# Kernel tuning notes

Hardware: AMD Instinct MI355X
Metric: run time of the kernel (lower is better)

## Reference

```python
import jax, jax.numpy as jnp
import numpy as np

N = 262144   # active voxel sites
C = 128      # channels (inplanes == outplanes)
K = 27       # 3^3 submanifold kernel offsets
EPS = 1e-4   # scn BatchNormalization default eps


def setup_inputs() -> dict:
    key = jax.random.key(0)
    ks = jax.random.split(key, 5)
    features = jax.random.normal(ks[0], (N, C), dtype=jnp.float32)
    nbr_idx = jax.random.randint(ks[1], (N, K), 0, N, dtype=jnp.int32)
    nbr_mask = jax.random.randint(ks[2], (N, K), 0, 2, dtype=jnp.int32)
    center = K // 2  # submanifold: center offset is always the site itself
    nbr_idx = nbr_idx.at[:, center].set(jnp.arange(N, dtype=jnp.int32))
    nbr_mask = nbr_mask.at[:, center].set(1)
    s = 1.0 / np.sqrt(K * C).astype(np.float32)
    W1 = jax.random.normal(ks[3], (K, C, C), dtype=jnp.float32) * s
    W2 = jax.random.normal(ks[4], (K, C, C), dtype=jnp.float32) * s
    bias1 = jnp.zeros((C,), jnp.float32)
    bias2 = jnp.zeros((C,), jnp.float32)
    gamma1 = jnp.ones((C,), jnp.float32)
    beta1 = jnp.zeros((C,), jnp.float32)
    gamma2 = jnp.ones((C,), jnp.float32)
    beta2 = jnp.zeros((C,), jnp.float32)
    return dict(features=features, nbr_idx=nbr_idx, nbr_mask=nbr_mask,
                gamma1=gamma1, beta1=beta1, W1=W1, bias1=bias1,
                gamma2=gamma2, beta2=beta2, W2=W2, bias2=bias2)


def _bn_relu(x, gamma, beta):
    # BatchNormReLU over active sites (training-mode batch stats)
    mu = jnp.mean(x, axis=0)
    var = jnp.mean(jnp.square(x - mu), axis=0)
    scale = gamma * jax.lax.rsqrt(var + EPS)
    return jax.nn.relu((x - mu) * scale + beta)


def _subm_conv(x, nbr_idx, nbr_mask, W, b):
    # Rulebook-based submanifold conv: for each of K offsets, gather the
    # active neighbor feature (masked) and apply that offset's [Cin,Cout] matmul.
    m = nbr_mask.astype(x.dtype)
    acc = jnp.broadcast_to(b, (x.shape[0], W.shape[2]))
    for k in range(K):  # fixed small unroll over kernel offsets
        g = x[nbr_idx[:, k]] * m[:, k:k + 1]   # [N, Cin]
        acc = acc + g @ W[k]                    # [N, Cout]
    return acc


def reference(features, nbr_idx, nbr_mask, gamma1, beta1, W1, bias1,
              gamma2, beta2, W2, bias2):
    h = _bn_relu(features, gamma1, beta1)
    h = _subm_conv(h, nbr_idx, nbr_mask, W1, bias1)
    h = _bn_relu(h, gamma2, beta2)
    h = _subm_conv(h, nbr_idx, nbr_mask, W2, bias2)
    return h + features  # AddTable residual
```

## Files before the change

### kernel.cpp

```cpp
#include <hip/hip_runtime.h>

#define NS 262144
#define NK 27

typedef float f32x4 __attribute__((ext_vector_type(4)));
typedef __bf16 bf16x8 __attribute__((ext_vector_type(8)));

__device__ __forceinline__ unsigned short f2bf(float f) {
  union { float f; unsigned int i; } c; c.f = f;
  unsigned int r = c.i + 0x7fffu + ((c.i >> 16) & 1u);
  return (unsigned short)(r >> 16);
}
__device__ __forceinline__ float bf2f(unsigned short u) {
  union { unsigned int i; float f; } c; c.i = ((unsigned int)u) << 16;
  return c.f;
}
__device__ __forceinline__ void async16(const void* gp, void* lp) {
  __builtin_amdgcn_global_load_lds((const __attribute__((address_space(1))) void*)gp,
                                   (__attribute__((address_space(3))) void*)lp, 16, 0, 0);
}

__global__ __launch_bounds__(256) void prep_idx_kernel(const int* __restrict__ nidx,
                                                       const int* __restrict__ nmask,
                                                       int* __restrict__ idx2t) {
  __shared__ int li[256 * NK];
  __shared__ int lm[256 * NK];
  const int t = threadIdx.x;
  const int sb = blockIdx.x * 256;
  for (int j = t; j < 256 * NK; j += 256) {
    li[j] = nidx[(size_t)sb * NK + j];
    lm[j] = nmask[(size_t)sb * NK + j];
  }
  __syncthreads();
  for (int k = 0; k < NK; ++k) {
    int m = lm[t * NK + k];
    int v = li[t * NK + k];
    idx2t[(size_t)k * NS + sb + t] = m ? v : NS;
  }
}

__global__ __launch_bounds__(256) void prep_w_kernel(const float* __restrict__ W1,
                                                     const float* __restrict__ W2,
                                                     unsigned short* __restrict__ Wt1,
                                                     unsigned short* __restrict__ Wt2) {
  const int b = blockIdx.x;
  const float* W = (b < NK) ? W1 : W2;
  unsigned short* Wt = (b < NK) ? Wt1 : Wt2;
  const int k = (b < NK) ? b : b - NK;
  __shared__ unsigned short tile[128 * 130];
  const int t = threadIdx.x;
  for (int j = t; j < 16384; j += 256) {
    int ci = j >> 7, co = j & 127;
    tile[ci * 130 + co] = f2bf(W[(size_t)k * 16384 + j]);
  }
  __syncthreads();
  for (int j = t; j < 16384; j += 256) {
    int co = j >> 7, ci = j & 127;
    Wt[(size_t)k * 16384 + j] = tile[ci * 130 + co];
  }
}

__global__ __launch_bounds__(256) void stats_kernel(const float* __restrict__ x,
                                                    float* __restrict__ ssum,
                                                    float* __restrict__ sssq) {
  const int t = threadIdx.x;
  const int c4 = (t & 31) * 4;
  const int rsub = t >> 5;
  const int rowend = blockIdx.x * 512 + 512;
  float s0 = 0, s1 = 0, s2 = 0, s3 = 0, q0 = 0, q1 = 0, q2 = 0, q3 = 0;
  for (int r = blockIdx.x * 512 + rsub; r < rowend; r += 8) {
    const float4 v = *(const float4*)&x[(size_t)r * 128 + c4];
    s0 += v.x; q0 += v.x * v.x;
    s1 += v.y; q1 += v.y * v.y;
    s2 += v.z; q2 += v.z * v.z;
    s3 += v.w; q3 += v.w * v.w;
  }
  __shared__ float red[256 * 8];
  red[t * 8 + 0] = s0; red[t * 8 + 1] = s1; red[t * 8 + 2] = s2; red[t * 8 + 3] = s3;
  red[t * 8 + 4] = q0; red[t * 8 + 5] = q1; red[t * 8 + 6] = q2; red[t * 8 + 7] = q3;
  __syncthreads();
  if (t < 32) {
    float a0 = 0, a1 = 0, a2 = 0, a3 = 0, b0 = 0, b1 = 0, b2 = 0, b3 = 0;
    for (int j = 0; j < 8; ++j) {
      const float* p = &red[(j * 32 + t) * 8];
      a0 += p[0]; a1 += p[1]; a2 += p[2]; a3 += p[3];
      b0 += p[4]; b1 += p[5]; b2 += p[6]; b3 += p[7];
    }
    atomicAdd(&ssum[t * 4 + 0], a0); atomicAdd(&ssum[t * 4 + 1], a1);
    atomicAdd(&ssum[t * 4 + 2], a2); atomicAdd(&ssum[t * 4 + 3], a3);
    atomicAdd(&sssq[t * 4 + 0], b0); atomicAdd(&sssq[t * 4 + 1], b1);
    atomicAdd(&sssq[t * 4 + 2], b2); atomicAdd(&sssq[t * 4 + 3], b3);
  }
}

__global__ __launch_bounds__(256) void apply_f32_kernel(const float* __restrict__ x,
    const float* __restrict__ ssum, const float* __restrict__ sssq,
    const float* __restrict__ gamma, const float* __restrict__ beta,
    unsigned short* __restrict__ hout) {
  const size_t base = ((size_t)blockIdx.x * 256 + threadIdx.x) * 8;
  const int c0 = (int)(base & 127);
  const float4 v0 = *(const float4*)&x[base];
  const float4 v1 = *(const float4*)&x[base + 4];
  const float vv[8] = {v0.x, v0.y, v0.z, v0.w, v1.x, v1.y, v1.z, v1.w};
  unsigned short o[8] __attribute__((aligned(16)));
  const float invN = 1.0f / (float)NS;
  #pragma unroll
  for (int j = 0; j < 8; ++j) {
    const int c = c0 + j;
    const float mean = ssum[c] * invN;
    const float var = sssq[c] * invN - mean * mean;
    const float sc = gamma[c] * rsqrtf(var + 1e-4f);
    const float t = (vv[j] - mean) * sc + beta[c];
    o[j] = f2bf(fmaxf(t, 0.0f));
  }
  *(int4*)&hout[base] = *(const int4*)o;
  if (blockIdx.x == 0 && threadIdx.x < 16) {
    int4 z; z.x = 0; z.y = 0; z.z = 0; z.w = 0;
    ((int4*)(hout + (size_t)NS * 128))[threadIdx.x] = z;
  }
}

__global__ __launch_bounds__(256) void apply_bf16_kernel(const unsigned short* __restrict__ x,
    const float* __restrict__ ssum, const float* __restrict__ sssq,
    const float* __restrict__ gamma, const float* __restrict__ beta,
    unsigned short* __restrict__ hout) {
  const size_t base = ((size_t)blockIdx.x * 256 + threadIdx.x) * 8;
  const int c0 = (int)(base & 127);
  unsigned short in[8] __attribute__((aligned(16)));
  *(int4*)in = *(const int4*)&x[base];
  unsigned short o[8] __attribute__((aligned(16)));
  const float invN = 1.0f / (float)NS;
  #pragma unroll
  for (int j = 0; j < 8; ++j) {
    const int c = c0 + j;
    const float mean = ssum[c] * invN;
    const float var = sssq[c] * invN - mean * mean;
    const float sc = gamma[c] * rsqrtf(var + 1e-4f);
    const float t = (bf2f(in[j]) - mean) * sc + beta[c];
    o[j] = f2bf(fmaxf(t, 0.0f));
  }
  *(int4*)&hout[base] = *(const int4*)o;
}


#define WAITV(N) asm volatile("s_waitcnt vmcnt(" #N ")" ::: "memory")
#define SBAR() do { __builtin_amdgcn_sched_barrier(0); __builtin_amdgcn_s_barrier(); \
                    __builtin_amdgcn_sched_barrier(0); } while (0)
#define ROT() do { int _t = b0; b0 = b1; b1 = b2; b2 = _t; } while (0)

#define LOAD_ROWS(KK, D0, D1) do {                                                   \
    D0 = idx2t[(size_t)(KK) * NS + sb + wave * 16 + rsel];                           \
    D1 = idx2t[(size_t)(KK) * NS + sb + 64 + wave * 16 + rsel];                      \
  } while (0)

#define STAGE_U(BS, KK, QQ, R0, R1) do {                                             \
    const unsigned short* ga0 = h + (((size_t)(R0)) << 7) + ((QQ) << 5) + (gch << 3);\
    async16(ga0, &A_lds[(BS) + (wave << 9)]);                                        \
    const unsigned short* gb0 = Wt + (((size_t)(KK)) << 14) +                        \
        ((wave * 16 + rsel) << 7) + ((QQ) << 5) + (gch << 3);                        \
    async16(gb0, &B_lds[(BS) + (wave << 9)]);                                        \
    const unsigned short* ga1 = h + (((size_t)(R1)) << 7) + ((QQ) << 5) + (gch << 3);\
    async16(ga1, &A_lds[(BS) + 2048 + (wave << 9)]);                                 \
    const unsigned short* gb1 = Wt + (((size_t)(KK)) << 14) +                        \
        ((64 + wave * 16 + rsel) << 7) + ((QQ) << 5) + (gch << 3);                   \
    async16(gb1, &B_lds[(BS) + 2048 + (wave << 9)]);                                 \
  } while (0)

#define COMPUTE_U(BS) do {                                                           \
    bf16x8 af[4], bfr[4];                                                            \
    _Pragma("unroll")                                                                \
    for (int mi = 0; mi < 4; ++mi)                                                   \
      af[mi] = *(const bf16x8*)&A_lds[(BS) + ((wm * 64 + mi * 16 + i16) << 5) + (slotc << 3)]; \
    _Pragma("unroll")                                                                \
    for (int ni = 0; ni < 4; ++ni)                                                   \
      bfr[ni] = *(const bf16x8*)&B_lds[(BS) + ((wn * 64 + ni * 16 + i16) << 5) + (slotc << 3)]; \
    __builtin_amdgcn_s_setprio(1);                                                   \
    _Pragma("unroll")                                                                \
    for (int mi = 0; mi < 4; ++mi)                                                   \
      _Pragma("unroll")                                                              \
      for (int ni = 0; ni < 4; ++ni)                                                 \
        acc[mi][ni] = __builtin_amdgcn_mfma_f32_16x16x32_bf16(af[mi], bfr[ni], acc[mi][ni], 0, 0, 0); \
    __builtin_amdgcn_s_setprio(0);                                                   \
  } while (0)

template <bool FIRST>
__global__ __launch_bounds__(256, 3) void conv_kernel(
    const unsigned short* __restrict__ h,
    const int* __restrict__ idx2t,
    const unsigned short* __restrict__ Wt,
    const float* __restrict__ bias,
    unsigned short* __restrict__ out_bf,
    float* __restrict__ ssum, float* __restrict__ sssq,
    const float* __restrict__ resid,
    float* __restrict__ outf) {
  __shared__ unsigned short A_lds[3 * 4096];
  __shared__ unsigned short B_lds[3 * 4096];
  const int tid = threadIdx.x;
  const int wave = tid >> 6, lane = tid & 63;
  const int wm = wave >> 1, wn = wave & 1;
  const int i16 = lane & 15, quad = lane >> 4;
  const int rsel = lane >> 2;
  const int gch = (lane & 3) ^ ((lane >> 3) & 3);
  const int slotc = quad ^ ((i16 >> 1) & 3);
  const int sb = blockIdx.x << 7;

  f32x4 acc[4][4];
  #pragma unroll
  for (int a = 0; a < 4; ++a)
    #pragma unroll
    for (int b = 0; b < 4; ++b) { acc[a][b][0] = 0.f; acc[a][b][1] = 0.f; acc[a][b][2] = 0.f; acc[a][b][3] = 0.f; }

  int rE0, rE1, rO0, rO1;
  LOAD_ROWS(0, rE0, rE1);
  LOAD_ROWS(1, rO0, rO1);
  int b0 = 0, b1 = 4096, b2 = 8192;
  STAGE_U(0, 0, 0, rE0, rE1);
  STAGE_U(4096, 0, 1, rE0, rE1);

  #pragma unroll 1
  for (int kk = 0; kk < 26; kk += 2) {
    STAGE_U(b2, kk, 2, rE0, rE1);                       WAITV(8);  SBAR(); COMPUTE_U(b0); SBAR(); ROT();
    STAGE_U(b2, kk, 3, rE0, rE1); LOAD_ROWS(kk + 2, rE0, rE1);
                                                        WAITV(10); SBAR(); COMPUTE_U(b0); SBAR(); ROT();
    STAGE_U(b2, kk + 1, 0, rO0, rO1);                   WAITV(10); SBAR(); COMPUTE_U(b0); SBAR(); ROT();
    STAGE_U(b2, kk + 1, 1, rO0, rO1);                   WAITV(8);  SBAR(); COMPUTE_U(b0); SBAR(); ROT();

    STAGE_U(b2, kk + 1, 2, rO0, rO1);                   WAITV(8);  SBAR(); COMPUTE_U(b0); SBAR(); ROT();
    { const int k3 = (kk + 3 > 26) ? 26 : kk + 3;
      STAGE_U(b2, kk + 1, 3, rO0, rO1); LOAD_ROWS(k3, rO0, rO1); }
                                                        WAITV(10); SBAR(); COMPUTE_U(b0); SBAR(); ROT();
    STAGE_U(b2, kk + 2, 0, rE0, rE1);                   WAITV(10); SBAR(); COMPUTE_U(b0); SBAR(); ROT();
    STAGE_U(b2, kk + 2, 1, rE0, rE1);                   WAITV(8);  SBAR(); COMPUTE_U(b0); SBAR(); ROT();
  }
  STAGE_U(b2, 26, 2, rE0, rE1);                         WAITV(8);  SBAR(); COMPUTE_U(b0); SBAR(); ROT();
  STAGE_U(b2, 26, 3, rE0, rE1);                         WAITV(8);  SBAR(); COMPUTE_U(b0); SBAR(); ROT();
                                                        WAITV(4);  SBAR(); COMPUTE_U(b0); SBAR(); ROT();
                                                        WAITV(0);  SBAR(); COMPUTE_U(b0); SBAR();

  if (FIRST) {
    float cs[4], cq[4];
    #pragma unroll
    for (int ni = 0; ni < 4; ++ni) {
      const int col = wn * 64 + ni * 16 + i16;
      const float bv = bias[col];
      float s = 0.f, q = 0.f;
      #pragma unroll
      for (int mi = 0; mi < 4; ++mi) {
        const int rowb = sb + wm * 64 + mi * 16 + quad * 4;
        #pragma unroll
        for (int i = 0; i < 4; ++i) {
          const float v = acc[mi][ni][i] + bv;
          out_bf[(size_t)(rowb + i) * 128 + col] = f2bf(v);
          s += v; q += v * v;
        }
      }
      cs[ni] = s; cq[ni] = q;
    }
    #pragma unroll
    for (int ni = 0; ni < 4; ++ni) {
      cs[ni] += __shfl_xor(cs[ni], 16); cs[ni] += __shfl_xor(cs[ni], 32);
      cq[ni] += __shfl_xor(cq[ni], 16); cq[ni] += __shfl_xor(cq[ni], 32);
    }
    __syncthreads();
    float* red = (float*)A_lds;
    if (wm == 1 && quad == 0) {
      #pragma unroll
      for (int ni = 0; ni < 4; ++ni) {
        const int col = wn * 64 + ni * 16 + i16;
        red[col] = cs[ni]; red[128 + col] = cq[ni];
      }
    }
    __syncthreads();
    if (wm == 0 && quad == 0) {
      #pragma unroll
      for (int ni = 0; ni < 4; ++ni) {
        const int col = wn * 64 + ni * 16 + i16;
        atomicAdd(&ssum[col], cs[ni] + red[col]);
        atomicAdd(&sssq[col], cq[ni] + red[128 + col]);
      }
    }
  } else {
    #pragma unroll
    for (int ni = 0; ni < 4; ++ni) {
      const int col = wn * 64 + ni * 16 + i16;
      const float bv = bias[col];
      #pragma unroll
      for (int mi = 0; mi < 4; ++mi) {
        const int rowb = sb + wm * 64 + mi * 16 + quad * 4;
        #pragma unroll
        for (int i = 0; i < 4; ++i) {
          const size_t o = (size_t)(rowb + i) * 128 + col;
          outf[o] = acc[mi][ni][i] + bv + resid[o];
        }
      }
    }
  }
}

extern "C" void kernel_launch(void* const* d_in, const int* in_sizes, int n_in,
                              void* d_out, int out_size, void* d_ws, size_t ws_size,
                              hipStream_t stream) {
  const float* features = (const float*)d_in[0];
  const int* nbr_idx    = (const int*)d_in[1];
  const int* nbr_mask   = (const int*)d_in[2];
  const float* gamma1   = (const float*)d_in[3];
  const float* beta1    = (const float*)d_in[4];
  const float* W1       = (const float*)d_in[5];
  const float* bias1    = (const float*)d_in[6];
  const float* gamma2   = (const float*)d_in[7];
  const float* beta2    = (const float*)d_in[8];
  const float* W2       = (const float*)d_in[9];
  const float* bias2    = (const float*)d_in[10];

  char* ws = (char*)d_ws;
  size_t off = 0;
  unsigned short* h = (unsigned short*)(ws + off); off += (size_t)(NS + 1) * 128 * 2;
  unsigned short* out1 = (unsigned short*)(ws + off); off += (size_t)NS * 128 * 2;
  int* idx2t = (int*)(ws + off); off += (size_t)NK * NS * 4;
  unsigned short* Wt1 = (unsigned short*)(ws + off); off += (size_t)NK * 128 * 128 * 2;
  unsigned short* Wt2 = (unsigned short*)(ws + off); off += (size_t)NK * 128 * 128 * 2;
  float* stats = (float*)(ws + off); off += 4 * 128 * 4;
  float* sum1 = stats, *ssq1 = stats + 128, *sum2 = stats + 256, *ssq2 = stats + 384;

  hipMemsetAsync(stats, 0, 4 * 128 * 4, stream);
  prep_idx_kernel<<<NS / 256, 256, 0, stream>>>(nbr_idx, nbr_mask, idx2t);
  prep_w_kernel<<<2 * NK, 256, 0, stream>>>(W1, W2, Wt1, Wt2);
  stats_kernel<<<NS / 512, 256, 0, stream>>>(features, sum1, ssq1);
  apply_f32_kernel<<<(NS * 128) / 2048, 256, 0, stream>>>(features, sum1, ssq1, gamma1, beta1, h);
  conv_kernel<true><<<NS / 128, 256, 0, stream>>>(h, idx2t, Wt1, bias1, out1, sum2, ssq2, nullptr, nullptr);
  apply_bf16_kernel<<<(NS * 128) / 2048, 256, 0, stream>>>(out1, sum2, ssq2, gamma2, beta2, h);
  conv_kernel<false><<<NS / 128, 256, 0, stream>>>(h, idx2t, Wt2, bias2, nullptr, nullptr, nullptr,
                                                   features, (float*)d_out);
}
```

Measured before the change: 943.6 us.

## Use one barrier per pipeline stage and issue staging before compute

Restructures the triple-buffered gather-GEMM loop so each stage waits for its own loads, takes a single barrier, issues the next async global-to-LDS stage, then computes on the current buffer. The second barrier per step goes away and row-index loads are issued just in time, which also lowers the vmcnt thresholds. Scheduling barriers pin the prologue issue order. This cuts barrier overhead and lets loads overlap the MFMA work, but it depends on the triple-buffer rotation keeping the buffer being written distinct from those being read.

Result: no change. 937.0 us (-0.7%).

```diff
diff --git a/kernel.cpp b/kernel.cpp
--- a/kernel.cpp
+++ b/kernel.cpp
@@ -143,7 +143,8 @@
 }
 
 
-#define WAITV(N) asm volatile("s_waitcnt vmcnt(" #N ")" ::: "memory")
+#define WAITV_(N) asm volatile("s_waitcnt vmcnt(" #N ")" ::: "memory")
+#define WAITV(N) WAITV_(N)
 #define SBAR() do { __builtin_amdgcn_sched_barrier(0); __builtin_amdgcn_s_barrier(); \
                     __builtin_amdgcn_sched_barrier(0); } while (0)
 #define ROT() do { int _t = b0; b0 = b1; b1 = b2; b2 = _t; } while (0)
@@ -212,30 +213,30 @@
 
   int rE0, rE1, rO0, rO1;
   LOAD_ROWS(0, rE0, rE1);
-  LOAD_ROWS(1, rO0, rO1);
+  __builtin_amdgcn_sched_barrier(0);
   int b0 = 0, b1 = 4096, b2 = 8192;
   STAGE_U(0, 0, 0, rE0, rE1);
+  __builtin_amdgcn_sched_barrier(0);
   STAGE_U(4096, 0, 1, rE0, rE1);
+  __builtin_amdgcn_sched_barrier(0);
 
   #pragma unroll 1
   for (int kk = 0; kk < 26; kk += 2) {
-    STAGE_U(b2, kk, 2, rE0, rE1);                       WAITV(8);  SBAR(); COMPUTE_U(b0); SBAR(); ROT();
-    STAGE_U(b2, kk, 3, rE0, rE1); LOAD_ROWS(kk + 2, rE0, rE1);
-                                                        WAITV(10); SBAR(); COMPUTE_U(b0); SBAR(); ROT();
-    STAGE_U(b2, kk + 1, 0, rO0, rO1);                   WAITV(10); SBAR(); COMPUTE_U(b0); SBAR(); ROT();
-    STAGE_U(b2, kk + 1, 1, rO0, rO1);                   WAITV(8);  SBAR(); COMPUTE_U(b0); SBAR(); ROT();
-
-    STAGE_U(b2, kk + 1, 2, rO0, rO1);                   WAITV(8);  SBAR(); COMPUTE_U(b0); SBAR(); ROT();
-    { const int k3 = (kk + 3 > 26) ? 26 : kk + 3;
-      STAGE_U(b2, kk + 1, 3, rO0, rO1); LOAD_ROWS(k3, rO0, rO1); }
-                                                        WAITV(10); SBAR(); COMPUTE_U(b0); SBAR(); ROT();
-    STAGE_U(b2, kk + 2, 0, rE0, rE1);                   WAITV(10); SBAR(); COMPUTE_U(b0); SBAR(); ROT();
-    STAGE_U(b2, kk + 2, 1, rE0, rE1);                   WAITV(8);  SBAR(); COMPUTE_U(b0); SBAR(); ROT();
-  }
-  STAGE_U(b2, 26, 2, rE0, rE1);                         WAITV(8);  SBAR(); COMPUTE_U(b0); SBAR(); ROT();
-  STAGE_U(b2, 26, 3, rE0, rE1);                         WAITV(8);  SBAR(); COMPUTE_U(b0); SBAR(); ROT();
-                                                        WAITV(4);  SBAR(); COMPUTE_U(b0); SBAR(); ROT();
-                                                        WAITV(0);  SBAR(); COMPUTE_U(b0); SBAR();
+    WAITV(4); SBAR(); STAGE_U(b2, kk, 2, rE0, rE1);     COMPUTE_U(b0); ROT();
+    WAITV(4); SBAR(); LOAD_ROWS(kk + 1, rO0, rO1);
+                      STAGE_U(b2, kk, 3, rE0, rE1);     COMPUTE_U(b0); ROT();
+    WAITV(6); SBAR(); STAGE_U(b2, kk + 1, 0, rO0, rO1); COMPUTE_U(b0); ROT();
+    WAITV(4); SBAR(); STAGE_U(b2, kk + 1, 1, rO0, rO1); COMPUTE_U(b0); ROT();
+    WAITV(4); SBAR(); STAGE_U(b2, kk + 1, 2, rO0, rO1); COMPUTE_U(b0); ROT();
+    WAITV(4); SBAR(); LOAD_ROWS(kk + 2, rE0, rE1);
+                      STAGE_U(b2, kk + 1, 3, rO0, rO1); COMPUTE_U(b0); ROT();
+    WAITV(6); SBAR(); STAGE_U(b2, kk + 2, 0, rE0, rE1); COMPUTE_U(b0); ROT();
+    WAITV(4); SBAR(); STAGE_U(b2, kk + 2, 1, rE0, rE1); COMPUTE_U(b0); ROT();
+  }
+  WAITV(4); SBAR(); STAGE_U(b2, 26, 2, rE0, rE1); COMPUTE_U(b0); ROT();
+  WAITV(4); SBAR(); STAGE_U(b2, 26, 3, rE0, rE1); COMPUTE_U(b0); ROT();
+  WAITV(4); SBAR(); COMPUTE_U(b0); ROT();
+  WAITV(0); SBAR(); COMPUTE_U(b0);
 
   if (FIRST) {
     float cs[4], cq[4];
```
